# Kernel tuning notes

Hardware: AMD Instinct MI355X
Metric: run time of the kernel (lower is better)

The kernel has to match this reference:

```python
import jax, jax.numpy as jnp
import numpy as np


def _split_feature(x, ns):
    # channel-last split: [b,h,w,c] -> [b*ns*ns, h/ns, w/ns, c]
    b, h, w, c = x.shape
    hn, wn = h // ns, w // ns
    return x.reshape(b, ns, hn, ns, wn, c).transpose(0, 1, 3, 2, 4, 5).reshape(b * ns * ns, hn, wn, c)


def _merge_splits(x, ns):
    # inverse of _split_feature: [b*ns*ns, h, w, c] -> [b, ns*h, ns*w, c]
    b, h, w, c = x.shape
    nb = b // (ns * ns)
    return x.reshape(nb, ns, ns, h, w, c).transpose(0, 1, 3, 2, 4, 5).reshape(nb, ns * h, ns * w, c)


def _gen_shift_window_attn_mask(h, w, ns):
    # numpy replica of _unimatch_generate_shift_window_attn_mask
    wsh, wsw = h // ns, w // ns
    ssh, ssw = wsh // 2, wsw // 2
    img = np.zeros((1, h, w, 1), dtype=np.float32)
    cnt = 0
    for hs in (slice(0, -wsh), slice(-wsh, -ssh), slice(-ssh, None)):
        for ws in (slice(0, -wsw), slice(-wsw, -ssw), slice(-ssw, None)):
            img[:, hs, ws, :] = cnt
            cnt += 1
    win = img.reshape(1, ns, wsh, ns, wsw, 1).transpose(0, 1, 3, 2, 4, 5).reshape(ns * ns, wsh * wsw)
    am = win[:, None, :] - win[:, :, None]
    return np.where(am != 0, np.float32(-100.0), np.float32(0.0)).astype(np.float32)


def setup_inputs() -> dict:
    key = jax.random.key(0)
    B, H, W, C, NS = 8, 96, 128, 128, 4
    kq, kk, kv = jax.random.split(key, 3)
    q = jax.random.normal(kq, (B, H * W, C), jnp.float32)
    k = jax.random.normal(kk, (B, H * W, C), jnp.float32)
    v = jax.random.normal(kv, (B, H * W, C), jnp.float32)
    attn_mask = jnp.asarray(_gen_shift_window_attn_mask(H, W, NS))  # [NS*NS, n, n]
    return {"q": q, "k": k, "v": v, "attn_mask": attn_mask,
            "num_splits": NS, "with_shift": 1, "h": H, "w": W}


def reference(q, k, v, attn_mask, num_splits, with_shift, h, w):
    b, _, c = q.shape
    ns = num_splits
    wsh, wsw = h // ns, w // ns
    n = wsh * wsw
    bn = b * ns * ns
    q = q.reshape(b, h, w, c)
    k = k.reshape(b, h, w, c)
    v = v.reshape(b, h, w, c)
    if with_shift:
        sh, sw = wsh // 2, wsw // 2
        q = jnp.roll(q, (-sh, -sw), axis=(1, 2))
        k = jnp.roll(k, (-sh, -sw), axis=(1, 2))
        v = jnp.roll(v, (-sh, -sw), axis=(1, 2))
    qf = _split_feature(q, ns).reshape(bn, n, c)
    kf = _split_feature(k, ns).reshape(bn, n, c)
    vf = _split_feature(v, ns).reshape(bn, n, c)
    scale = jnp.asarray(c, qf.dtype) ** 0.5
    scores = jnp.einsum('bnc,bmc->bnm', qf, kf) / scale  # [bn, n, n]
    if with_shift:
        scores = scores + jnp.tile(attn_mask, (b, 1, 1))
    attn = jax.nn.softmax(scores, axis=-1)
    out = jnp.einsum('bnm,bmc->bnc', attn, vf)
    out = _merge_splits(out.reshape(bn, wsh, wsw, c), ns)  # [b, h, w, c]
    if with_shift:
        out = jnp.roll(out, (sh, sw), axis=(1, 2))
    return out.reshape(b, h * w, c)
```

## Files before the change

### kernel.cpp

```cpp
#include <hip/hip_runtime.h>

#define H 96
#define W 128
#define C 128
#define WSH 24
#define WSW 32
#define NTOK 768
#define SH 12
#define SW 16
#define KT 32
#define NKT 24
#define TILE_USH 8192
#define WS_NEED (128L * NKT * TILE_USH * 2)

typedef __attribute__((ext_vector_type(8))) short short8;
typedef __attribute__((ext_vector_type(4))) float floatx4;

union U8 { short8 s8; unsigned u[4]; };

__device__ inline unsigned short f2bf(float f) {
  union { float f; unsigned u; } un; un.f = f;
  unsigned r = un.u + 0x7FFF + ((un.u >> 16) & 1);
  return (unsigned short)(r >> 16);
}

__device__ inline int tok_off(int tok, int wh, int ww) {
  int r = tok >> 5;
  int cc = tok & 31;
  int y = wh * WSH + r + SH; if (y >= H) y -= H;
  int x = ww * WSW + cc + SW; if (x >= W) x -= W;
  return y * W + x;
}

__device__ inline void gll16(const void* g, void* lds) {
  __builtin_amdgcn_global_load_lds(
      (const __attribute__((address_space(1))) unsigned int*)g,
      (__attribute__((address_space(3))) unsigned int*)lds, 16, 0, 0);
}

__global__ __launch_bounds__(256) void prep_kernel(const float* __restrict__ k,
                                                   const float* __restrict__ v,
                                                   unsigned short* __restrict__ ws) {
  __shared__ unsigned short Vlds[KT][136];
  const int bid = blockIdx.x;
  const int xcd = bid & 7;
  const int jj = bid >> 3;
  const int w = xcd * 16 + (jj & 15);
  const int kt = jj >> 4;
  const int batch = w >> 4, win = w & 15;
  const int wh = win >> 2, ww = win & 3;
  int y = wh * WSH + kt + SH; if (y >= H) y -= H;

  const int t = threadIdx.x;
  const int key = t >> 3;
  const int j = t & 7;
  const int c0 = j * 16;
  int x = ww * WSW + key + SW; if (x >= W) x -= W;
  const long src = ((long)batch * H * W + (long)y * W + x) * C + c0;
  unsigned short* tile = ws + ((long)w * NKT + kt) * TILE_USH;

  {
    const float* kp = k + src;
    short8 s0, s1;
#pragma unroll
    for (int i = 0; i < 2; ++i) {
      floatx4 a = *(const floatx4*)(kp + i * 8);
      floatx4 b = *(const floatx4*)(kp + i * 8 + 4);
      s0[i*4+0] = (short)f2bf(a[0]); s0[i*4+1] = (short)f2bf(a[1]);
      s0[i*4+2] = (short)f2bf(a[2]); s0[i*4+3] = (short)f2bf(a[3]);
      s1[i*4+0] = (short)f2bf(b[0]); s1[i*4+1] = (short)f2bf(b[1]);
      s1[i*4+2] = (short)f2bf(b[2]); s1[i*4+3] = (short)f2bf(b[3]);
    }
    short8 o0, o1;
    o0[0]=s0[0]; o0[1]=s0[1]; o0[2]=s0[2]; o0[3]=s0[3]; o0[4]=s1[0]; o0[5]=s1[1]; o0[6]=s1[2]; o0[7]=s1[3];
    o1[0]=s0[4]; o1[1]=s0[5]; o1[2]=s0[6]; o1[3]=s0[7]; o1[4]=s1[4]; o1[5]=s1[5]; o1[6]=s1[6]; o1[7]=s1[7];
    const int kc = j >> 1;
    const int q2 = (j & 1) * 2;
    const int half = key >> 4, keyh = key & 15;
    unsigned short* kout = tile + kc * 1024 + half * 512 + keyh * 8;
    *(short8*)(kout + (q2    ) * 128) = o0;
    *(short8*)(kout + (q2 + 1) * 128) = o1;
  }
  {
    const float* vp = v + src;
#pragma unroll
    for (int i = 0; i < 4; ++i) {
      floatx4 a = *(const floatx4*)(vp + i * 4);
      unsigned lo = (unsigned)f2bf(a[0]) | ((unsigned)f2bf(a[1]) << 16);
      unsigned hi = (unsigned)f2bf(a[2]) | ((unsigned)f2bf(a[3]) << 16);
      *(unsigned*)&Vlds[key][c0 + i*4]     = lo;
      *(unsigned*)&Vlds[key][c0 + i*4 + 2] = hi;
    }
  }
  __syncthreads();
  {
    const int cb = t >> 5;
    const int rem = t & 31;
    const int col = rem >> 1, qh = rem & 1;
    const int ch = cb * 16 + col;
#pragma unroll
    for (int qs = 0; qs < 2; ++qs) {
      const int quad = qh * 2 + qs;
      short8 o;
#pragma unroll
      for (int i = 0; i < 8; ++i)
        o[i] = (short)Vlds[(i & 1) * 16 + quad * 4 + (i >> 1)][ch];
      *(short8*)(tile + 4096 + cb * 512 + (quad * 16 + col) * 8) = o;
    }
  }
}

__global__ __launch_bounds__(256, 3) void attn_main(const float* __restrict__ q,
                                                    const unsigned short* __restrict__ ws,
                                                    float* __restrict__ out) {
  __shared__ unsigned short Kv[3][TILE_USH];

  const int bid = blockIdx.x;
  const int x8 = bid & 7;
  const int i = bid >> 3;
  const int w = x8 * 16 + (i & 15);
  const int qb = i >> 4;
  const int batch = w >> 4, win = w & 15;
  const int wh = win >> 2, ww = win & 3;

  const int tid = threadIdx.x;
  const int wv = tid >> 6, lane = tid & 63;
  const int col = lane & 15, quad = lane >> 4;
  const long bbase = (long)batch * (H * W * C);
  const int qbase = qb * 128 + wv * 32;
  const int loff = lane * 8;

  const char* wtile = (const char*)(ws + (long)w * (NKT * TILE_USH));

  auto stage = [&](int buf, int kt) {
    const char* g = wtile + ((long)kt << 14);
#pragma unroll
    for (int c = 0; c < 4; ++c) {
      const int chunk = wv * 4 + c;
      gll16(g + chunk * 1024 + lane * 16, &Kv[buf][chunk * 512]);
    }
  };

  stage(0, 0); stage(1, 1); stage(2, 2);

  short8 qfrag[2][4];
#pragma unroll
  for (int s = 0; s < 2; ++s) {
    const int qtok = qbase + s * 16 + col;
    const float* qp = q + bbase + (long)tok_off(qtok, wh, ww) * C + quad * 8;
#pragma unroll
    for (int kc = 0; kc < 4; ++kc) {
      floatx4 a = *(const floatx4*)(qp + kc * 32);
      floatx4 b = *(const floatx4*)(qp + kc * 32 + 4);
      short8 v8;
      v8[0]=(short)f2bf(a[0]); v8[1]=(short)f2bf(a[1]); v8[2]=(short)f2bf(a[2]); v8[3]=(short)f2bf(a[3]);
      v8[4]=(short)f2bf(b[0]); v8[5]=(short)f2bf(b[1]); v8[6]=(short)f2bf(b[2]); v8[7]=(short)f2bf(b[3]);
      qfrag[s][kc] = v8;
    }
  }

  int qreg[2];
#pragma unroll
  for (int s = 0; s < 2; ++s) {
    int t0 = qbase + s * 16;
    int rr_s = t0 >> 5;
    int qh = (wh == 3) ? ((rr_s >= SH) ? 2 : 1) : 0;
    int qw = (ww == 3) ? ((t0 & 16) ? 2 : 1) : 0;
    qreg[s] = qh * 3 + qw;
  }
  const int cw0 = (ww == 3) ? 1 : 0, cw1 = (ww == 3) ? 2 : 0;
  const float MNEG = -144.2695041f;
  const float SC2 = 0.12751739f;

  floatx4 oacc[2][8];
#pragma unroll
  for (int s = 0; s < 2; ++s)
#pragma unroll
    for (int cb = 0; cb < 8; ++cb) oacc[s][cb] = (floatx4){0.f, 0.f, 0.f, 0.f};
  float lsum[2] = {0.f, 0.f};

  short8 pfc[2];
  short8 vf[8];

  auto qk_sm = [&](int kt, int buf) {
    short8 kf0[4], kf1[4];
#pragma unroll
    for (int kc = 0; kc < 4; ++kc) {
      kf0[kc] = *(const short8*)&Kv[buf][kc * 1024 + loff];
      kf1[kc] = *(const short8*)&Kv[buf][kc * 1024 + 512 + loff];
    }
    const int khb = (wh == 3) ? ((kt >= SH) ? 6 : 3) : 0;
    const int kr0 = khb + cw0, kr1 = khb + cw1;

    floatx4 A0[2], A1[2];
#pragma unroll
    for (int s = 0; s < 2; ++s) {
      A0[s] = (floatx4){0.f, 0.f, 0.f, 0.f};
      A1[s] = (floatx4){0.f, 0.f, 0.f, 0.f};
    }
    __builtin_amdgcn_s_setprio(1);
#pragma unroll
    for (int kc = 0; kc < 4; ++kc)
#pragma unroll
      for (int s = 0; s < 2; ++s) {
        A0[s] = __builtin_amdgcn_mfma_f32_16x16x32_bf16(kf0[kc], qfrag[s][kc], A0[s], 0, 0, 0);
        A1[s] = __builtin_amdgcn_mfma_f32_16x16x32_bf16(kf1[kc], qfrag[s][kc], A1[s], 0, 0, 0);
      }
    __builtin_amdgcn_s_setprio(0);

#pragma unroll
    for (int s = 0; s < 2; ++s) {
      const float m0 = (qreg[s] == kr0) ? 0.f : MNEG;
      const float m1 = (qreg[s] == kr1) ? 0.f : MNEG;
      float ls = 0.f;
      U8 pk;
#pragma unroll
      for (int r = 0; r < 4; ++r) {
        float p0 = __builtin_amdgcn_exp2f(fmaf(A0[s][r], SC2, m0));
        float p1 = __builtin_amdgcn_exp2f(fmaf(A1[s][r], SC2, m1));
        ls += p0 + p1;
        pk.u[r] = (unsigned)f2bf(p0) | ((unsigned)f2bf(p1) << 16);
      }
      lsum[s] += ls;
      pfc[s] = pk.s8;
    }
  };

  auto loadV = [&](int buf) {
#pragma unroll
    for (int cb = 0; cb < 8; ++cb)
      vf[cb] = *(const short8*)&Kv[buf][4096 + cb * 512 + loff];
  };
  auto pv = [&]() {
    __builtin_amdgcn_s_setprio(1);
#pragma unroll
    for (int cb = 0; cb < 8; ++cb)
#pragma unroll
      for (int s = 0; s < 2; ++s)
        oacc[s][cb] = __builtin_amdgcn_mfma_f32_16x16x32_bf16(pfc[s], vf[cb], oacc[s][cb], 0, 0, 0);
    __builtin_amdgcn_s_setprio(0);
  };

  asm volatile("s_waitcnt vmcnt(8)" ::: "memory");
  __builtin_amdgcn_s_barrier();

  qk_sm(0, 0);
  loadV(0);
  asm volatile("s_waitcnt vmcnt(4) lgkmcnt(0)" ::: "memory");
  __builtin_amdgcn_s_barrier();

  for (int kt = 1; kt < NKT; ++kt) {
    const int buf = kt % 3;
    if (kt + 2 < NKT) stage((kt + 2) % 3, kt + 2);

    pv();
    qk_sm(kt, buf);
    loadV(buf);

    if (kt + 1 < NKT) {
      if (kt + 2 < NKT) asm volatile("s_waitcnt vmcnt(4) lgkmcnt(0)" ::: "memory");
      else              asm volatile("s_waitcnt vmcnt(0) lgkmcnt(0)" ::: "memory");
      __builtin_amdgcn_s_barrier();
    }
  }
  pv();

#pragma unroll
  for (int s = 0; s < 2; ++s) {
    float l = lsum[s];
    l += __shfl_xor(l, 16);
    l += __shfl_xor(l, 32);
#pragma unroll
    for (int r = 0; r < 4; ++r) {
      float lr = __shfl(l, quad * 4 + r);
      float inv = 1.0f / lr;
      int tok = qbase + s * 16 + quad * 4 + r;
      float* op = out + bbase + (long)tok_off(tok, wh, ww) * C + col;
#pragma unroll
      for (int cb = 0; cb < 8; ++cb) op[cb * 16] = oacc[s][cb][r] * inv;
    }
  }
}

#define KSTRF 136
#define VSTRF 40
#define PSTRF 40
__global__ __launch_bounds__(256, 2) void attn_fallback(
    const float* __restrict__ q, const float* __restrict__ k,
    const float* __restrict__ v, const float* __restrict__ mask,
    float* __restrict__ out) {
  __shared__ unsigned short Ks[KT * KSTRF];
  __shared__ unsigned short Vtl[C * VSTRF];
  __shared__ unsigned short Psf[4][16 * PSTRF];
  const int qtile = blockIdx.x;
  const int beta  = blockIdx.y;
  const int batch = beta >> 4;
  const int win   = beta & 15;
  const int wh = win >> 2, ww = win & 3;
  const int tid = threadIdx.x;
  const int wave = tid >> 6, lane = tid & 63;
  const int col = lane & 15, quad = lane >> 4;
  const long bbase = (long)batch * (H * W * C);
  const int qtok = qtile * 64 + wave * 16 + col;
  const float* qp = q + bbase + (long)tok_off(qtok, wh, ww) * C + quad * 8;
  short8 qfrag[4];
#pragma unroll
  for (int kc = 0; kc < 4; ++kc) {
    floatx4 a = *(const floatx4*)(qp + kc * 32);
    floatx4 b = *(const floatx4*)(qp + kc * 32 + 4);
    short8 s;
    s[0]=f2bf(a[0]); s[1]=f2bf(a[1]); s[2]=f2bf(a[2]); s[3]=f2bf(a[3]);
    s[4]=f2bf(b[0]); s[5]=f2bf(b[1]); s[6]=f2bf(b[2]); s[7]=f2bf(b[3]);
    qfrag[kc] = s;
  }
  floatx4 oacc[8];
#pragma unroll
  for (int i = 0; i < 8; ++i) oacc[i] = (floatx4){0.f,0.f,0.f,0.f};
  float mrow[4], lrow[4];
#pragma unroll
  for (int r = 0; r < 4; ++r) { mrow[r] = -1e30f; lrow[r] = 0.f; }
  const int skey = tid >> 3;
  const int sch  = (tid & 7) * 4;
  const float invscale = 0.088388347648318447f;
  const float* maskw = mask + (long)win * (NTOK * NTOK);
  const int qrow_m = qtile * 64 + wave * 16 + quad * 4;
  for (int kt = 0; kt < NKT; ++kt) {
    const int ktok0 = kt * KT;
    const long srow = bbase + (long)tok_off(ktok0 + skey, wh, ww) * C;
    const float* kp = k + srow;
    const float* vp = v + srow;
    __syncthreads();
#pragma unroll
    for (int j = 0; j < 4; ++j) {
      floatx4 f = *(const floatx4*)(kp + sch + j * 32);
      unsigned lo = (unsigned)f2bf(f[0]) | ((unsigned)f2bf(f[1]) << 16);
      unsigned hi = (unsigned)f2bf(f[2]) | ((unsigned)f2bf(f[3]) << 16);
      *(uint2*)&Ks[skey * KSTRF + sch + j * 32] = make_uint2(lo, hi);
    }
#pragma unroll
    for (int j = 0; j < 4; ++j) {
      floatx4 f = *(const floatx4*)(vp + sch + j * 32);
      int chb = sch + j * 32;
      Vtl[(chb + 0) * VSTRF + skey] = f2bf(f[0]);
      Vtl[(chb + 1) * VSTRF + skey] = f2bf(f[1]);
      Vtl[(chb + 2) * VSTRF + skey] = f2bf(f[2]);
      Vtl[(chb + 3) * VSTRF + skey] = f2bf(f[3]);
    }
    __syncthreads();
    floatx4 s0 = (floatx4){0.f,0.f,0.f,0.f};
    floatx4 s1 = (floatx4){0.f,0.f,0.f,0.f};
#pragma unroll
    for (int kc = 0; kc < 4; ++kc) {
      short8 k0 = *(const short8*)&Ks[col * KSTRF + kc * 32 + quad * 8];
      short8 k1 = *(const short8*)&Ks[(col + 16) * KSTRF + kc * 32 + quad * 8];
      s0 = __builtin_amdgcn_mfma_f32_16x16x32_bf16(qfrag[kc], k0, s0, 0, 0, 0);
      s1 = __builtin_amdgcn_mfma_f32_16x16x32_bf16(qfrag[kc], k1, s1, 0, 0, 0);
    }
    float mk0[4], mk1[4];
    const float* mp = maskw + (long)qrow_m * NTOK + ktok0 + col;
#pragma unroll
    for (int r = 0; r < 4; ++r) { mk0[r] = mp[r * NTOK]; mk1[r] = mp[r * NTOK + 16]; }
#pragma unroll
    for (int r = 0; r < 4; ++r) {
      float a0 = s0[r] * invscale + mk0[r];
      float a1 = s1[r] * invscale + mk1[r];
      float mx = fmaxf(a0, a1);
      mx = fmaxf(mx, __shfl_xor(mx, 1)); mx = fmaxf(mx, __shfl_xor(mx, 2));
      mx = fmaxf(mx, __shfl_xor(mx, 4)); mx = fmaxf(mx, __shfl_xor(mx, 8));
      float mnew = fmaxf(mrow[r], mx);
      float alpha = __expf(mrow[r] - mnew);
      float p0 = __expf(a0 - mnew);
      float p1 = __expf(a1 - mnew);
      float rs = p0 + p1;
      rs += __shfl_xor(rs, 1); rs += __shfl_xor(rs, 2);
      rs += __shfl_xor(rs, 4); rs += __shfl_xor(rs, 8);
      lrow[r] = lrow[r] * alpha + rs;
      mrow[r] = mnew;
#pragma unroll
      for (int cb = 0; cb < 8; ++cb) oacc[cb][r] *= alpha;
      Psf[wave][(quad * 4 + r) * PSTRF + col]      = f2bf(p0);
      Psf[wave][(quad * 4 + r) * PSTRF + 16 + col] = f2bf(p1);
    }
    __syncthreads();
    short8 pf = *(const short8*)&Psf[wave][col * PSTRF + quad * 8];
#pragma unroll
    for (int cb = 0; cb < 8; ++cb) {
      short8 vf = *(const short8*)&Vtl[(cb * 16 + col) * VSTRF + quad * 8];
      oacc[cb] = __builtin_amdgcn_mfma_f32_16x16x32_bf16(pf, vf, oacc[cb], 0, 0, 0);
    }
  }
#pragma unroll
  for (int r = 0; r < 4; ++r) {
    float inv_l = 1.0f / lrow[r];
    int tok = qtile * 64 + wave * 16 + quad * 4 + r;
    float* op = out + bbase + (long)tok_off(tok, wh, ww) * C + col;
#pragma unroll
    for (int cb = 0; cb < 8; ++cb) op[cb * 16] = oacc[cb][r] * inv_l;
  }
}

extern "C" void kernel_launch(void* const* d_in, const int* in_sizes, int n_in,
                              void* d_out, int out_size, void* d_ws, size_t ws_size,
                              hipStream_t stream) {
  const float* q    = (const float*)d_in[0];
  const float* k    = (const float*)d_in[1];
  const float* v    = (const float*)d_in[2];
  const float* mask = (const float*)d_in[3];
  float* out = (float*)d_out;
  if (ws_size >= (size_t)WS_NEED) {
    prep_kernel<<<128 * NKT, 256, 0, stream>>>(k, v, (unsigned short*)d_ws);
    attn_main<<<768, 256, 0, stream>>>(q, (const unsigned short*)d_ws, out);
  } else {
    attn_fallback<<<dim3(12, 128), dim3(256), 0, stream>>>(q, k, v, mask, out);
  }
}
```

Measured before the change: 241.6 us.

## Halve query rows per block, double-buffer K/V, and raise occupancy

Each wave now handles 16 query rows instead of 32, so the grid doubles to 1536 blocks and register use drops. The K/V LDS ring shrinks from three buffers to two, and launch bounds target four blocks per CU. The software-pipelined PV/QK interleave becomes a simple per-tile loop with a barrier before the next stage is issued. The aim is more latency hiding through occupancy. The cost is twice the K/V traffic from the workspace, less per-wave MFMA ILP, an extra barrier per tile, and a partial final wave of blocks.

Measured after the change: 253.2 us. 1.05x slower.

```diff
diff --git a/kernel.cpp b/kernel.cpp
--- a/kernel.cpp
+++ b/kernel.cpp
@@ -110,10 +110,10 @@
   }
 }
 
-__global__ __launch_bounds__(256, 3) void attn_main(const float* __restrict__ q,
+__global__ __launch_bounds__(256, 4) void attn_main(const float* __restrict__ q,
                                                     const unsigned short* __restrict__ ws,
                                                     float* __restrict__ out) {
-  __shared__ unsigned short Kv[3][TILE_USH];
+  __shared__ unsigned short Kv[2][TILE_USH];
 
   const int bid = blockIdx.x;
   const int x8 = bid & 7;
@@ -127,7 +127,7 @@
   const int wv = tid >> 6, lane = tid & 63;
   const int col = lane & 15, quad = lane >> 4;
   const long bbase = (long)batch * (H * W * C);
-  const int qbase = qb * 128 + wv * 32;
+  const int qbase = qb * 64 + wv * 16;
   const int loff = lane * 8;
 
   const char* wtile = (const char*)(ws + (long)w * (NKT * TILE_USH));
@@ -141,12 +141,11 @@
     }
   };
 
-  stage(0, 0); stage(1, 1); stage(2, 2);
-
-  short8 qfrag[2][4];
-#pragma unroll
-  for (int s = 0; s < 2; ++s) {
-    const int qtok = qbase + s * 16 + col;
+  stage(0, 0); stage(1, 1);
+
+  short8 qfrag[4];
+  {
+    const int qtok = qbase + col;
     const float* qp = q + bbase + (long)tok_off(qtok, wh, ww) * C + quad * 8;
 #pragma unroll
     for (int kc = 0; kc < 4; ++kc) {
@@ -155,129 +154,97 @@
       short8 v8;
       v8[0]=(short)f2bf(a[0]); v8[1]=(short)f2bf(a[1]); v8[2]=(short)f2bf(a[2]); v8[3]=(short)f2bf(a[3]);
       v8[4]=(short)f2bf(b[0]); v8[5]=(short)f2bf(b[1]); v8[6]=(short)f2bf(b[2]); v8[7]=(short)f2bf(b[3]);
-      qfrag[s][kc] = v8;
-    }
-  }
-
-  int qreg[2];
-#pragma unroll
-  for (int s = 0; s < 2; ++s) {
-    int t0 = qbase + s * 16;
+      qfrag[kc] = v8;
+    }
+  }
+
+  int qreg;
+  {
+    int t0 = qbase;
     int rr_s = t0 >> 5;
     int qh = (wh == 3) ? ((rr_s >= SH) ? 2 : 1) : 0;
     int qw = (ww == 3) ? ((t0 & 16) ? 2 : 1) : 0;
-    qreg[s] = qh * 3 + qw;
+    qreg = qh * 3 + qw;
   }
   const int cw0 = (ww == 3) ? 1 : 0, cw1 = (ww == 3) ? 2 : 0;
   const float MNEG = -144.2695041f;
   const float SC2 = 0.12751739f;
 
-  floatx4 oacc[2][8];
-#pragma unroll
-  for (int s = 0; s < 2; ++s)
-#pragma unroll
-    for (int cb = 0; cb < 8; ++cb) oacc[s][cb] = (floatx4){0.f, 0.f, 0.f, 0.f};
-  float lsum[2] = {0.f, 0.f};
-
-  short8 pfc[2];
-  short8 vf[8];
-
-  auto qk_sm = [&](int kt, int buf) {
-    short8 kf0[4], kf1[4];
+  floatx4 oacc[8];
+#pragma unroll
+  for (int cb = 0; cb < 8; ++cb) oacc[cb] = (floatx4){0.f, 0.f, 0.f, 0.f};
+  float lsum = 0.f;
+
+  asm volatile("s_waitcnt vmcnt(4)" ::: "memory");
+  __builtin_amdgcn_s_barrier();
+
+  for (int kt = 0; kt < NKT; ++kt) {
+    const int buf = kt & 1;
+
+    short8 kf0[4], kf1[4], vf[8];
 #pragma unroll
     for (int kc = 0; kc < 4; ++kc) {
       kf0[kc] = *(const short8*)&Kv[buf][kc * 1024 + loff];
       kf1[kc] = *(const short8*)&Kv[buf][kc * 1024 + 512 + loff];
     }
+#pragma unroll
+    for (int cb = 0; cb < 8; ++cb)
+      vf[cb] = *(const short8*)&Kv[buf][4096 + cb * 512 + loff];
+
+    asm volatile("s_waitcnt lgkmcnt(0)" ::: "memory");
+    __builtin_amdgcn_s_barrier();
+    if (kt + 2 < NKT) stage(buf, kt + 2);
+
     const int khb = (wh == 3) ? ((kt >= SH) ? 6 : 3) : 0;
     const int kr0 = khb + cw0, kr1 = khb + cw1;
-
-    floatx4 A0[2], A1[2];
-#pragma unroll
-    for (int s = 0; s < 2; ++s) {
-      A0[s] = (floatx4){0.f, 0.f, 0.f, 0.f};
-      A1[s] = (floatx4){0.f, 0.f, 0.f, 0.f};
-    }
+    floatx4 A0 = (floatx4){0.f, 0.f, 0.f, 0.f};
+    floatx4 A1 = (floatx4){0.f, 0.f, 0.f, 0.f};
     __builtin_amdgcn_s_setprio(1);
 #pragma unroll
-    for (int kc = 0; kc < 4; ++kc)
-#pragma unroll
-      for (int s = 0; s < 2; ++s) {
-        A0[s] = __builtin_amdgcn_mfma_f32_16x16x32_bf16(kf0[kc], qfrag[s][kc], A0[s], 0, 0, 0);
-        A1[s] = __builtin_amdgcn_mfma_f32_16x16x32_bf16(kf1[kc], qfrag[s][kc], A1[s], 0, 0, 0);
-      }
+    for (int kc = 0; kc < 4; ++kc) {
+      A0 = __builtin_amdgcn_mfma_f32_16x16x32_bf16(kf0[kc], qfrag[kc], A0, 0, 0, 0);
+      A1 = __builtin_amdgcn_mfma_f32_16x16x32_bf16(kf1[kc], qfrag[kc], A1, 0, 0, 0);
+    }
     __builtin_amdgcn_s_setprio(0);
 
-#pragma unroll
-    for (int s = 0; s < 2; ++s) {
-      const float m0 = (qreg[s] == kr0) ? 0.f : MNEG;
-      const float m1 = (qreg[s] == kr1) ? 0.f : MNEG;
-      float ls = 0.f;
-      U8 pk;
-#pragma unroll
-      for (int r = 0; r < 4; ++r) {
-        float p0 = __builtin_amdgcn_exp2f(fmaf(A0[s][r], SC2, m0));
-        float p1 = __builtin_amdgcn_exp2f(fmaf(A1[s][r], SC2, m1));
-        ls += p0 + p1;
-        pk.u[r] = (unsigned)f2bf(p0) | ((unsigned)f2bf(p1) << 16);
-      }
-      lsum[s] += ls;
-      pfc[s] = pk.s8;
-    }
-  };
-
-  auto loadV = [&](int buf) {
+    const float m0 = (qreg == kr0) ? 0.f : MNEG;
+    const float m1 = (qreg == kr1) ? 0.f : MNEG;
+    float ls = 0.f;
+    U8 pk;
+#pragma unroll
+    for (int r = 0; r < 4; ++r) {
+      float p0 = __builtin_amdgcn_exp2f(fmaf(A0[r], SC2, m0));
+      float p1 = __builtin_amdgcn_exp2f(fmaf(A1[r], SC2, m1));
+      ls += p0 + p1;
+      pk.u[r] = (unsigned)f2bf(p0) | ((unsigned)f2bf(p1) << 16);
+    }
+    lsum += ls;
+
+    __builtin_amdgcn_s_setprio(1);
 #pragma unroll
     for (int cb = 0; cb < 8; ++cb)
-      vf[cb] = *(const short8*)&Kv[buf][4096 + cb * 512 + loff];
-  };
-  auto pv = [&]() {
-    __builtin_amdgcn_s_setprio(1);
-#pragma unroll
-    for (int cb = 0; cb < 8; ++cb)
-#pragma unroll
-      for (int s = 0; s < 2; ++s)
-        oacc[s][cb] = __builtin_amdgcn_mfma_f32_16x16x32_bf16(pfc[s], vf[cb], oacc[s][cb], 0, 0, 0);
+      oacc[cb] = __builtin_amdgcn_mfma_f32_16x16x32_bf16(pk.s8, vf[cb], oacc[cb], 0, 0, 0);
     __builtin_amdgcn_s_setprio(0);
-  };
-
-  asm volatile("s_waitcnt vmcnt(8)" ::: "memory");
-  __builtin_amdgcn_s_barrier();
-
-  qk_sm(0, 0);
-  loadV(0);
-  asm volatile("s_waitcnt vmcnt(4) lgkmcnt(0)" ::: "memory");
-  __builtin_amdgcn_s_barrier();
-
-  for (int kt = 1; kt < NKT; ++kt) {
-    const int buf = kt % 3;
-    if (kt + 2 < NKT) stage((kt + 2) % 3, kt + 2);
-
-    pv();
-    qk_sm(kt, buf);
-    loadV(buf);
 
     if (kt + 1 < NKT) {
-      if (kt + 2 < NKT) asm volatile("s_waitcnt vmcnt(4) lgkmcnt(0)" ::: "memory");
-      else              asm volatile("s_waitcnt vmcnt(0) lgkmcnt(0)" ::: "memory");
+      if (kt + 2 < NKT) asm volatile("s_waitcnt vmcnt(4)" ::: "memory");
+      else              asm volatile("s_waitcnt vmcnt(0)" ::: "memory");
       __builtin_amdgcn_s_barrier();
     }
   }
-  pv();
-
-#pragma unroll
-  for (int s = 0; s < 2; ++s) {
-    float l = lsum[s];
+
+  {
+    float l = lsum;
     l += __shfl_xor(l, 16);
     l += __shfl_xor(l, 32);
 #pragma unroll
     for (int r = 0; r < 4; ++r) {
       float lr = __shfl(l, quad * 4 + r);
       float inv = 1.0f / lr;
-      int tok = qbase + s * 16 + quad * 4 + r;
+      int tok = qbase + quad * 4 + r;
       float* op = out + bbase + (long)tok_off(tok, wh, ww) * C + col;
 #pragma unroll
-      for (int cb = 0; cb < 8; ++cb) op[cb * 16] = oacc[s][cb][r] * inv;
+      for (int cb = 0; cb < 8; ++cb) op[cb * 16] = oacc[cb][r] * inv;
     }
   }
 }
@@ -409,7 +376,7 @@
   float* out = (float*)d_out;
   if (ws_size >= (size_t)WS_NEED) {
     prep_kernel<<<128 * NKT, 256, 0, stream>>>(k, v, (unsigned short*)d_ws);
-    attn_main<<<768, 256, 0, stream>>>(q, (const unsigned short*)d_ws, out);
+    attn_main<<<1536, 256, 0, stream>>>(q, (const unsigned short*)d_ws, out);
   } else {
     attn_fallback<<<dim3(12, 128), dim3(256), 0, stream>>>(q, k, v, mask, out);
   }
```
